# Performance work log

Hardware: AMD Instinct MI355X
Metric: run time of the kernel (lower is better)

The kernel has to match this reference:

```python
import jax, jax.numpy as jnp
import numpy as np
from jax import lax

K = 3           # number of channel clusters (hard-coded in the torch forward)
KM_ITERS = 50   # fixed Lloyd iterations (stand-in for sklearn KMeans, random_state=0)

SEQ_LEN, PRED_LEN, CH, BATCH = 1024, 192, 1000, 32
LH = SEQ_LEN // 2


def _pairwise_sqdist(z, c):
    # z: [N, D], c: [K, D] -> [N, K]
    zz = jnp.sum(z * z, axis=1, keepdims=True)          # [N,1]
    cc = jnp.sum(c * c, axis=1)[None, :]                # [1,K]
    return zz - 2.0 * (z @ c.T) + cc


def kmeans_labels(z, k=K, iters=KM_ITERS):
    # Deterministic Lloyd's algorithm; init = first k rows (deterministic stand-in
    # for sklearn's k-means++ with random_state=0).
    c0 = z[:k]

    def step(c, _):
        d = _pairwise_sqdist(z, c)
        labels = jnp.argmin(d, axis=1)
        ones = jnp.ones((z.shape[0],), z.dtype)
        sums = jax.ops.segment_sum(z, labels, num_segments=k)       # [K,D]
        counts = jax.ops.segment_sum(ones, labels, num_segments=k)  # [K]
        new_c = jnp.where(counts[:, None] > 0,
                          sums / jnp.maximum(counts, 1.0)[:, None], c)
        return new_c, None

    c, _ = lax.scan(step, c0, None, length=iters)
    return jnp.argmin(_pairwise_sqdist(z, c), axis=1)   # [N] int32


def setup_inputs() -> dict:
    key = jax.random.key(0)
    ks = jax.random.split(key, 4)
    x = jax.random.normal(ks[0], (BATCH, SEQ_LEN, CH), dtype=jnp.float32)
    # stacked per-cluster expert Linears g1/g2/g3: weight [K, P, Lh], bias [K, P]
    Wg = jax.random.normal(ks[1], (K, PRED_LEN, LH), dtype=jnp.float32) * 0.02
    bg = jnp.zeros((K, PRED_LEN), dtype=jnp.float32)
    Wu = jax.random.normal(ks[2], (PRED_LEN, LH), dtype=jnp.float32) * 0.02
    bu = jnp.zeros((PRED_LEN,), dtype=jnp.float32)
    z1 = jnp.zeros((1,), dtype=jnp.float32)
    return {"x": x, "x_mark_enc": z1, "x_dec": z1, "x_mark_dec": z1,
            "Wg": Wg, "bg": bg, "Wu": Wu, "bu": bu}


def reference(x, x_mark_enc, x_dec, x_mark_dec, Wg, bg, Wu, bu):
    # instance normalization over time (torch.var is unbiased -> ddof=1)
    x_mean = jnp.mean(x, axis=1, keepdims=True)
    xc = x - x_mean
    x_var = jnp.var(xc, axis=1, keepdims=True, ddof=1) + 1e-5
    xn = xc / jnp.sqrt(x_var)

    # Haar split along time
    x1 = xn[:, 0::2, :] * 0.5
    x2 = xn[:, 1::2, :] * 0.5
    x_L = x1 + x2          # [B, Lh, N]
    x_U = x1 - x2          # [B, Lh, N]

    # channel clustering on z = x_L reshaped to [N, B*Lh]
    B, Lh, N = x_L.shape
    z = x_L.reshape(B * Lh, N).T                      # [N, B*Lh]
    labels = kmeans_labels(z)                         # [N]

    # per-cluster Linear experts expressed as per-channel gathered weights
    # (identical math to gather g_k -> g_kLinear -> scatter back)
    Wn = Wg[labels]                                   # [N, P, Lh]
    bn = bg[labels]                                   # [N, P]
    g = jnp.einsum('bln,npl->bpn', x_L, Wn) + bn.T[None]   # [B, P, N]

    xu = jnp.einsum('bln,pl->bpn', x_U, Wu) + bu[None, :, None]

    xy = xu + g
    return xy * jnp.sqrt(x_var) + x_mean
```

## Files before the change

kernel.cpp:

```cpp
#include <hip/hip_runtime.h>
#include <hip/hip_bf16.h>
#include <hip/hip_cooperative_groups.h>

namespace cg = cooperative_groups;

#define B_   32
#define L_   1024
#define LH_  512
#define CH_  1000
#define PRED_ 192
#define ITERS_ 50
#define KBL_ 16384
#define SLOTS_ 1012
#define NTILES_ 253
#define NT2_ 506
#define NTRI_ 36
#define SEG_ 16
#define KMB_ 32
#define KMP_ 32

typedef __attribute__((ext_vector_type(8))) _Float16 f16x8;
typedef __attribute__((ext_vector_type(4))) float f32x4;

__device__ inline ushort f2h(float x) {
    union { _Float16 h; ushort u; } c;
    c.h = (_Float16)x;
    return c.u;
}

__global__ __launch_bounds__(256) void k1_partial(const float* __restrict__ x,
                                                  float* __restrict__ pS,
                                                  float* __restrict__ pSS) {
    int seg = blockIdx.x;
    int b = blockIdx.y;
    int t = threadIdx.x;
    if (t >= 250) return;
    int c4 = t * 4;
    const float* xp = x + (size_t)b * L_ * CH_ + (size_t)seg * 64 * CH_ + c4;
    float4 s = {0.f, 0.f, 0.f, 0.f}, ss = {0.f, 0.f, 0.f, 0.f};
#pragma unroll 4
    for (int l = 0; l < 64; ++l) {
        float4 v = *(const float4*)(xp + (size_t)l * CH_);
        s.x += v.x; s.y += v.y; s.z += v.z; s.w += v.w;
        ss.x += v.x * v.x; ss.y += v.y * v.y; ss.z += v.z * v.z; ss.w += v.w * v.w;
    }
    size_t o = ((size_t)seg * B_ + b) * CH_ + c4;
    *(float4*)(pS + o) = s;
    *(float4*)(pSS + o) = ss;
}

__global__ __launch_bounds__(256) void k1b_wprep(const float* __restrict__ pS,
                                                 const float* __restrict__ pSS,
                                                 float* __restrict__ meanT,
                                                 float* __restrict__ sstdT,
                                                 float* __restrict__ invT,
                                                 const float* __restrict__ Wg,
                                                 const float* __restrict__ Wu,
                                                 ushort* __restrict__ WF2) {
    int bx = blockIdx.x;
    int tid = threadIdx.x;
    if (bx < 125) {
        int idx = bx * 256 + tid;
        if (idx >= B_ * CH_) return;
        int c = idx % CH_;
        int b = idx / CH_;
        float s = 0.f, ss = 0.f;
#pragma unroll
        for (int seg = 0; seg < SEG_; ++seg) {
            size_t o = ((size_t)seg * B_ + b) * CH_ + c;
            s += pS[o];
            ss += pSS[o];
        }
        float m = s * (1.0f / L_);
        float var = (ss - (float)L_ * m * m) * (1.0f / (L_ - 1)) + 1e-5f;
        float sd = sqrtf(var);
        meanT[c * B_ + b] = m;
        sstdT[c * B_ + b] = sd;
        invT[c * B_ + b] = 1.0f / sd;
    } else {
        int r = bx - 125;
        int p = r % PRED_;
#pragma unroll
        for (int i = 0; i < 4; ++i) {
            int k = i * 256 + tid;
            float w = (k < 512) ? Wg[(size_t)r * LH_ + k]
                                : Wu[(size_t)p * LH_ + (k - 512)];
            WF2[(size_t)r * 1024 + k] = f2h(w);
        }
    }
}

__global__ __launch_bounds__(256) void k2_build(const float* __restrict__ x,
                                                const float* __restrict__ meanT,
                                                const float* __restrict__ invT,
                                                ushort* __restrict__ zLF,
                                                ushort* __restrict__ zUF) {
    __shared__ float Ls[32][33];
    __shared__ float Us[32][33];
    int tid = threadIdx.x;
    int tx = tid & 31, ty = tid >> 5;
    int n0 = blockIdx.x * 32;
    int lh0 = blockIdx.y * 32;
    int b = blockIdx.z;
    int n = n0 + tx;
    float m = 0.f, iv = 0.f;
    if (n < CH_) { m = meanT[n * B_ + b]; iv = invT[n * B_ + b]; }
    for (int r = 0; r < 4; ++r) {
        int lh = lh0 + ty + 8 * r;
        float v0 = 0.f, v1 = 0.f;
        if (n < CH_) {
            v0 = x[((size_t)b * L_ + 2 * lh) * CH_ + n];
            v1 = x[((size_t)b * L_ + 2 * lh + 1) * CH_ + n];
        }
        float a = (v0 - m) * iv * 0.5f;
        float c2 = (v1 - m) * iv * 0.5f;
        Ls[ty + 8 * r][tx] = a + c2;
        Us[ty + 8 * r][tx] = a - c2;
    }
    __syncthreads();
    for (int r = 0; r < 4; ++r) {
        int nl = ty + 8 * r;
        int nn = n0 + nl;
        if (nn < CH_) {
            size_t dst = (size_t)nn * KBL_ + (size_t)b * LH_ + lh0 + tx;
            zLF[dst] = f2h(Ls[tx][nl]);
            zUF[dst] = f2h(Us[tx][nl]);
        }
    }
}

#define ZSPLIT_ 16
#define KSEG_   1024
#define NT_     (KSEG_ / 32)

__global__ __launch_bounds__(256) void k3_mfma(const ushort* __restrict__ zF,
                                               float* __restrict__ gpart) {
    __shared__ __align__(16) ushort AH[128][40];
    __shared__ __align__(16) ushort BH[128][40];

    int bid = blockIdx.x;
    int xcd = bid & 7, w = bid >> 3;
    int ksl = 2 * xcd + (w >= NTRI_);
    int t = (w >= NTRI_) ? w - NTRI_ : w;
    int ti = 0, tt = t;
    while (tt >= 8 - ti) { tt -= 8 - ti; ++ti; }
    int tj = ti + tt;
    int i0 = ti * 128, j0 = tj * 128;
    int kb = ksl * KSEG_;

    int tid = threadIdx.x;
    int lane = tid & 63;
    int wid = tid >> 6;
    int wr = wid >> 1, wc = wid & 1;
    int fr = lane & 15;
    int g8 = lane >> 4;

    f32x4 acc[4][4];
#pragma unroll
    for (int m = 0; m < 4; ++m)
#pragma unroll
        for (int n = 0; n < 4; ++n) acc[m][n] = (f32x4){0.f, 0.f, 0.f, 0.f};

    int srow = tid >> 2;
    int sseg = tid & 3;

    uint4 pv[4];
    auto stage_load = [&](int kt) {
        int k0 = kb + kt * 32;
#pragma unroll
        for (int s = 0; s < 4; ++s) {
            int tile = s >> 1, rep = s & 1;
            int row = srow + rep * 64;
            int grow = ((tile == 0) ? i0 : j0) + row;
            uint4 v = {0u, 0u, 0u, 0u};
            if (grow < CH_)
                v = *(const uint4*)(zF + (size_t)grow * KBL_ + k0 + sseg * 8);
            pv[s] = v;
        }
    };
    auto stage_write = [&]() {
#pragma unroll
        for (int s = 0; s < 4; ++s) {
            int tile = s >> 1, rep = s & 1;
            int row = srow + rep * 64;
            ushort* dst = (tile == 0) ? &AH[row][sseg * 8] : &BH[row][sseg * 8];
            *(uint4*)dst = pv[s];
        }
    };

    stage_load(0);
    for (int t2 = 0; t2 < NT_; ++t2) {
        __syncthreads();
        stage_write();
        __syncthreads();
        if (t2 + 1 < NT_) stage_load(t2 + 1);

        f16x8 a[4];
#pragma unroll
        for (int m = 0; m < 4; ++m)
            a[m] = *(const f16x8*)&AH[wr * 64 + m * 16 + fr][g8 * 8];
#pragma unroll
        for (int n = 0; n < 4; ++n) {
            f16x8 bv = *(const f16x8*)&BH[wc * 64 + n * 16 + fr][g8 * 8];
#pragma unroll
            for (int m = 0; m < 4; ++m)
                acc[m][n] = __builtin_amdgcn_mfma_f32_16x16x32_f16(a[m], bv, acc[m][n], 0, 0, 0);
        }
    }

    float* gp = gpart + ((size_t)ksl * NTRI_ + t) * 16384;
#pragma unroll
    for (int m = 0; m < 4; ++m) {
        int rb = wr * 64 + m * 16 + g8 * 4;
#pragma unroll
        for (int n = 0; n < 4; ++n) {
            int c = wc * 64 + n * 16 + fr;
#pragma unroll
            for (int q = 0; q < 4; ++q)
                gp[(size_t)(rb + q) * 128 + c] = acc[m][n][q];
        }
    }
}

__global__ __launch_bounds__(256) void k3b_sym(const float* __restrict__ gpart,
                                               float* __restrict__ g) {
    int t = blockIdx.x;
    int seg = blockIdx.y;
    int ti = 0, tt = t;
    while (tt >= 8 - ti) { tt -= 8 - ti; ++ti; }
    int tj = ti + tt;
    int i0 = ti * 128, j0 = tj * 128;
    int tid = threadIdx.x;
    int e0 = seg * 4096 + tid * 16;
    int r = e0 >> 7, c0 = e0 & 127;

    float4 s[4];
#pragma unroll
    for (int j = 0; j < 4; ++j) s[j] = (float4){0.f, 0.f, 0.f, 0.f};
#pragma unroll
    for (int p = 0; p < ZSPLIT_; ++p) {
        const float* src = gpart + ((size_t)p * NTRI_ + t) * 16384 + e0;
#pragma unroll
        for (int j = 0; j < 4; ++j) {
            float4 v = *(const float4*)(src + j * 4);
            s[j].x += v.x; s[j].y += v.y; s[j].z += v.z; s[j].w += v.w;
        }
    }
    int i = i0 + r;
    if (i < CH_) {
#pragma unroll
        for (int j = 0; j < 4; ++j) {
            int jc = j0 + c0 + j * 4;
            if (jc + 3 < CH_) {
                *(float4*)(g + (size_t)i * CH_ + jc) = s[j];
            } else {
#pragma unroll
                for (int e = 0; e < 4; ++e)
                    if (jc + e < CH_) g[(size_t)i * CH_ + jc + e] = ((const float*)&s[j])[e];
            }
        }
        if (ti != tj) {
#pragma unroll
            for (int j = 0; j < 4; ++j) {
#pragma unroll
                for (int e = 0; e < 4; ++e) {
                    int jc = j0 + c0 + j * 4 + e;
                    if (jc < CH_) g[(size_t)jc * CH_ + i] = ((const float*)&s[j])[e];
                }
            }
        }
    }
}

__global__ __launch_bounds__(1024) void k4_kmeans(const float* __restrict__ g,
                                                  float* __restrict__ sbuf,
                                                  int* __restrict__ chlist,
                                                  int* __restrict__ chpos,
                                                  int* __restrict__ slabel) {
    cg::grid_group grid = cg::this_grid();
    __shared__ float gl[KMP_ * CH_];
    __shared__ int   lab[1024];
    __shared__ float wred[16][3];
    __shared__ float ccS[3];
    __shared__ float ccPrev[3];
    __shared__ int   cntPrev[3];
    __shared__ int   cnt2[3];
    __shared__ int   chgS;
    __shared__ int   st[4], c2r[3];

    int tid = threadIdx.x;
    int wv = tid >> 6, ln64 = tid & 63;
    int bpt0 = blockIdx.x * KMP_;

    {
        int nrow = CH_ - bpt0;
        if (nrow > KMP_) nrow = KMP_;
        if (nrow < 0) nrow = 0;
        int nf4 = nrow * (CH_ / 4);
        const float4* gsrc = (const float4*)(g + (size_t)bpt0 * CH_);
        float4* gdst = (float4*)gl;
        for (int i = tid; i < nf4; i += 1024) gdst[i] = gsrc[i];
    }

    int lbp = (tid < 3) ? tid : 3;
    lab[tid] = lbp;
    if (tid < 3) {
        cntPrev[tid] = 1;
        ccPrev[tid] = g[(size_t)tid * CH_ + tid];
    }
    __syncthreads();

    int par = 0;
    for (int it = 1; it <= ITERS_ + 1; ++it) {
        const float* sp = sbuf + par * 3 * CH_;
        float s0 = 0.f, s1 = 0.f, s2 = 0.f;
        if (tid < CH_) {
            if (it == 1) {
                const float* gr = g + (size_t)tid * CH_;
                s0 = gr[0]; s1 = gr[1]; s2 = gr[2];
            } else {
                s0 = sp[tid * 3 + 0]; s1 = sp[tid * 3 + 1]; s2 = sp[tid * 3 + 2];
            }
        }
        float c0 = (lbp == 0) ? s0 : 0.f;
        float c1 = (lbp == 1) ? s1 : 0.f;
        float c2 = (lbp == 2) ? s2 : 0.f;
#pragma unroll
        for (int m = 1; m < 64; m <<= 1) {
            c0 += __shfl_xor(c0, m);
            c1 += __shfl_xor(c1, m);
            c2 += __shfl_xor(c2, m);
        }
        if (ln64 == 0) { wred[wv][0] = c0; wred[wv][1] = c1; wred[wv][2] = c2; }
        if (tid == 0) { cnt2[0] = 0; cnt2[1] = 0; cnt2[2] = 0; chgS = 0; }
        __syncthreads();
        if (tid < 3) {
            float sacc = 0.f;
#pragma unroll
            for (int w2 = 0; w2 < 16; ++w2) sacc += wred[w2][tid];
            int n = cntPrev[tid];
            float cc = (n > 0) ? sacc / (float)n : ccPrev[tid];
            ccS[tid] = cc;
            ccPrev[tid] = cc;
        }
        __syncthreads();
        float cc0 = ccS[0], cc1 = ccS[1], cc2 = ccS[2];

        int nl = lbp;
        if (tid < CH_) {
            float d0 = cc0 - 2.f * s0;
            float d1 = cc1 - 2.f * s1;
            float d2 = cc2 - 2.f * s2;
            nl = 0; float dm = d0;
            if (d1 < dm) { dm = d1; nl = 1; }
            if (d2 < dm) { dm = d2; nl = 2; }
        }
        bool act = (tid < CH_);
        unsigned long long b0 = __ballot(act && nl == 0);
        unsigned long long b1 = __ballot(act && nl == 1);
        unsigned long long b2 = __ballot(act && nl == 2);
        unsigned long long bc = __ballot(act && nl != lbp);
        if (ln64 == 0) {
            if (b0) atomicAdd(&cnt2[0], (int)__popcll(b0));
            if (b1) atomicAdd(&cnt2[1], (int)__popcll(b1));
            if (b2) atomicAdd(&cnt2[2], (int)__popcll(b2));
            if (bc) atomicAdd(&chgS, (int)__popcll(bc));
        }
        lab[tid] = nl;
        lbp = nl;
        __syncthreads();

        if (it == ITERS_ + 1) break;
        if (chgS == 0 && it > 1) break;

        int n0n = cnt2[0], n1n = cnt2[1], n2n = cnt2[2];
        float* sq = sbuf + (par ^ 1) * 3 * CH_;
        int pl = tid >> 5;
        int ln = tid & 31;
        int i = bpt0 + pl;
        if (i < CH_) {
            const float* gr = gl + pl * CH_;
            float a0 = 0.f, a1 = 0.f, a2 = 0.f;
            for (int j = ln; j < CH_; j += 32) {
                float gv = gr[j];
                int lb = lab[j];
                a0 += (lb == 0) ? gv : 0.f;
                a1 += (lb == 1) ? gv : 0.f;
                a2 += (lb == 2) ? gv : 0.f;
            }
#pragma unroll
            for (int msk = 1; msk < 32; msk <<= 1) {
                a0 += __shfl_xor(a0, msk, 32);
                a1 += __shfl_xor(a1, msk, 32);
                a2 += __shfl_xor(a2, msk, 32);
            }
            if (ln == 0) {
                float f0, f1, f2;
                if (it == 1) { f0 = gr[0]; f1 = gr[1]; f2 = gr[2]; }
                else { f0 = sp[i * 3 + 0]; f1 = sp[i * 3 + 1]; f2 = sp[i * 3 + 2]; }
                sq[i * 3 + 0] = (n0n > 0) ? a0 / (float)n0n : f0;
                sq[i * 3 + 1] = (n1n > 0) ? a1 / (float)n1n : f1;
                sq[i * 3 + 2] = (n2n > 0) ? a2 / (float)n2n : f2;
            }
        }
        if (tid < 3) cntPrev[tid] = cnt2[tid];
        par ^= 1;
        grid.sync();
    }

    if (blockIdx.x == 0) {
        if (tid == 0) {
            st[0] = 0;
            st[1] = ((cnt2[0] + 3) >> 2) << 2;
            st[2] = st[1] + (((cnt2[1] + 3) >> 2) << 2);
            st[3] = st[2] + (((cnt2[2] + 3) >> 2) << 2);
            c2r[0] = 0; c2r[1] = 0; c2r[2] = 0;
        }
        __syncthreads();
        if (tid < SLOTS_) chlist[tid] = 0;
        if (tid < NTILES_) {
            int s = tid * 4;
            slabel[tid] = (s < st[1]) ? 0 : (s < st[2]) ? 1 : (s < st[3]) ? 2 : 0;
        }
        __syncthreads();
        if (tid < CH_) {
            int lb = lab[tid];
            int r = atomicAdd(&c2r[lb], 1);
            int slot = st[lb] + r;
            chlist[slot] = tid;
            chpos[tid] = slot;
        }
    }
}

__global__ __launch_bounds__(256) void k5_grouped(const ushort* __restrict__ zLF,
                                                  const ushort* __restrict__ zUF,
                                                  const ushort* __restrict__ WF2,
                                                  const int* __restrict__ chlist,
                                                  const int* __restrict__ slabel,
                                                  const float* __restrict__ bg,
                                                  const float* __restrict__ bu,
                                                  const float* __restrict__ meanT,
                                                  const float* __restrict__ sstdT,
                                                  float* __restrict__ outP) {
    __shared__ __align__(16) ushort ZT[64][40];
    __shared__ __align__(16) ushort WT[192][40];
    __shared__ int sch[2];

    int tile = blockIdx.x;
    int tid = threadIdx.x;
    if (tid < 2) sch[tid] = chlist[tile * 2 + tid];
    int lab = slabel[tile >> 1];
    __syncthreads();

    int lane = tid & 63, wid = tid >> 6;
    int fr = lane & 15, g8 = lane >> 4;

    int srow = tid >> 2, sseg = tid & 3;
    size_t zb = (size_t)sch[srow >> 5] * KBL_ + (size_t)(srow & 31) * LH_;
    const ushort* wbase = WF2 + (size_t)(lab * PRED_) * 1024;

    f32x4 acc[4][3];
#pragma unroll
    for (int m = 0; m < 4; ++m)
#pragma unroll
        for (int n = 0; n < 3; ++n) acc[m][n] = (f32x4){0.f, 0.f, 0.f, 0.f};

    uint4 pz, pw0, pw1, pw2;
    auto stage_load = [&](int t) {
        const ushort* zsrc = (t < 16) ? zLF : zUF;
        int ko = ((t & 15) * 32) + sseg * 8;
        pz  = *(const uint4*)(zsrc + zb + ko);
        int kw = t * 32 + sseg * 8;
        pw0 = *(const uint4*)(wbase + (size_t)srow * 1024 + kw);
        pw1 = *(const uint4*)(wbase + (size_t)(srow + 64) * 1024 + kw);
        pw2 = *(const uint4*)(wbase + (size_t)(srow + 128) * 1024 + kw);
    };
    auto stage_write = [&]() {
        *(uint4*)&ZT[srow][sseg * 8] = pz;
        *(uint4*)&WT[srow][sseg * 8] = pw0;
        *(uint4*)&WT[srow + 64][sseg * 8] = pw1;
        *(uint4*)&WT[srow + 128][sseg * 8] = pw2;
    };

    stage_load(0);
    for (int t = 0; t < 32; ++t) {
        __syncthreads();
        stage_write();
        __syncthreads();
        if (t + 1 < 32) stage_load(t + 1);

        f16x8 a[4];
#pragma unroll
        for (int m = 0; m < 4; ++m)
            a[m] = *(const f16x8*)&ZT[m * 16 + fr][g8 * 8];
#pragma unroll
        for (int nf = 0; nf < 3; ++nf) {
            f16x8 bv = *(const f16x8*)&WT[wid * 48 + nf * 16 + fr][g8 * 8];
#pragma unroll
            for (int m = 0; m < 4; ++m)
                acc[m][nf] = __builtin_amdgcn_mfma_f32_16x16x32_f16(a[m], bv, acc[m][nf], 0, 0, 0);
        }
    }

#pragma unroll
    for (int m = 0; m < 4; ++m) {
#pragma unroll
        for (int q = 0; q < 4; ++q) {
            int sb = m * 16 + g8 * 4 + q;
            int sl = sb >> 5, b = sb & 31;
            int n = sch[sl];
            float sd = sstdT[n * B_ + b], mu = meanT[n * B_ + b];
            size_t obase = ((size_t)(tile * 2 + sl) * B_ + b) * PRED_;
#pragma unroll
            for (int nf = 0; nf < 3; ++nf) {
                int p = wid * 48 + nf * 16 + fr;
                float v = acc[m][nf][q] + bg[lab * PRED_ + p] + bu[p];
                outP[obase + p] = v * sd + mu;
            }
        }
    }
}

__global__ __launch_bounds__(256) void k7_unperm(const float* __restrict__ outP,
                                                 const int* __restrict__ chpos,
                                                 float* __restrict__ out) {
    int n = blockIdx.x * 256 + threadIdx.x;
    int p0 = blockIdx.y * 32;
    int b = blockIdx.z;
    if (n >= CH_) return;
    const float* src = outP + ((size_t)chpos[n] * B_ + b) * PRED_ + p0;
    float4 v[8];
#pragma unroll
    for (int j = 0; j < 8; ++j) v[j] = *(const float4*)(src + j * 4);
#pragma unroll
    for (int j = 0; j < 8; ++j) {
#pragma unroll
        for (int e = 0; e < 4; ++e) {
            int p = p0 + j * 4 + e;
            out[((size_t)b * PRED_ + p) * CH_ + n] = ((const float*)&v[j])[e];
        }
    }
}

extern "C" void kernel_launch(void* const* d_in, const int* in_sizes, int n_in,
                              void* d_out, int out_size, void* d_ws, size_t ws_size,
                              hipStream_t stream) {
    const float* x  = (const float*)d_in[0];
    const float* Wg = (const float*)d_in[4];
    const float* bg = (const float*)d_in[5];
    const float* Wu = (const float*)d_in[6];
    const float* bu = (const float*)d_in[7];
    float* out = (float*)d_out;
    (void)in_sizes; (void)n_in; (void)out_size; (void)ws_size;

    char* ws = (char*)d_ws;
    size_t off = 0;
    auto alloc = [&](size_t bytes) {
        void* p = ws + off;
        off = (off + bytes + 255) & ~(size_t)255;
        return p;
    };
    ushort* zLF  = (ushort*)alloc((size_t)16384000 * 2);
    ushort* zUF  = (ushort*)alloc((size_t)16384000 * 2);
    float*  G    = (float*)alloc((size_t)1000000 * 4);
    ushort* WF2  = (ushort*)alloc((size_t)576 * 1024 * 2);
    float*  meanT = (float*)alloc((size_t)32000 * 4);
    float*  sstdT = (float*)alloc((size_t)32000 * 4);
    float*  invT  = (float*)alloc((size_t)32000 * 4);
    float*  pS   = (float*)alloc((size_t)SEG_ * B_ * CH_ * 4);
    float*  pSS  = (float*)alloc((size_t)SEG_ * B_ * CH_ * 4);
    float*  sbuf = (float*)alloc((size_t)2 * 3 * CH_ * 4);
    int*    chlist = (int*)alloc((size_t)SLOTS_ * 4);
    int*    chpos  = (int*)alloc((size_t)1024 * 4);
    int*    slabel = (int*)alloc((size_t)256 * 4);
    char* unionBase = (char*)alloc((size_t)ZSPLIT_ * NTRI_ * 16384 * 4);
    float* Gp   = (float*)unionBase;
    float* outP = (float*)unionBase;

    k1_partial<<<dim3(SEG_, 32), 256, 0, stream>>>(x, pS, pSS);
    k1b_wprep<<<125 + 576, 256, 0, stream>>>(pS, pSS, meanT, sstdT, invT, Wg, Wu, WF2);
    k2_build<<<dim3(32, 16, 32), 256, 0, stream>>>(x, meanT, invT, zLF, zUF);
    k3_mfma<<<8 * NTRI_ * 2, 256, 0, stream>>>(zLF, Gp);
    k3b_sym<<<dim3(NTRI_, 4), 256, 0, stream>>>(Gp, G);
    void* args[] = { (void*)&G, (void*)&sbuf, (void*)&chlist, (void*)&chpos, (void*)&slabel };
    hipLaunchCooperativeKernel((void*)k4_kmeans, dim3(KMB_), dim3(1024), args, 0, stream);
    k5_grouped<<<NT2_, 256, 0, stream>>>(zLF, zUF, WF2, chlist, slabel,
                                         bg, bu, meanT, sstdT, outP);
    k7_unperm<<<dim3(4, 6, 32), 256, 0, stream>>>(outP, chpos, out);
}
```

Before: 199.4 us.

## Fuse split-K reduction into MFMA kernel via last-block atomic counter

The separate symmetric reduction kernel is removed. Each Gram tile's split-K partials are now reduced by the last of its 16 blocks to finish, which it detects with an atomic counter and threadfences. The weight fp16 conversion also moves into the partial-sum kernel, so it runs alongside the statistics pass rather than alongside the mean/std reduce. This cuts kernel-launch gaps, at the cost of an extra memset launch and a serialized tail where a single block per tile does the whole reduction.

```diff
diff --git a/kernel.cpp b/kernel.cpp
--- a/kernel.cpp
+++ b/kernel.cpp
@@ -28,66 +28,65 @@
     return c.u;
 }
 
-__global__ __launch_bounds__(256) void k1_partial(const float* __restrict__ x,
-                                                  float* __restrict__ pS,
-                                                  float* __restrict__ pSS) {
-    int seg = blockIdx.x;
-    int b = blockIdx.y;
+__global__ __launch_bounds__(256) void k1_fused(const float* __restrict__ x,
+                                                float* __restrict__ pS,
+                                                float* __restrict__ pSS,
+                                                const float* __restrict__ Wg,
+                                                const float* __restrict__ Wu,
+                                                ushort* __restrict__ WF2) {
+    int bx = blockIdx.x;
     int t = threadIdx.x;
-    if (t >= 250) return;
-    int c4 = t * 4;
-    const float* xp = x + (size_t)b * L_ * CH_ + (size_t)seg * 64 * CH_ + c4;
-    float4 s = {0.f, 0.f, 0.f, 0.f}, ss = {0.f, 0.f, 0.f, 0.f};
+    if (bx < 512) {
+        int seg = bx & 15;
+        int b = bx >> 4;
+        if (t >= 250) return;
+        int c4 = t * 4;
+        const float* xp = x + (size_t)b * L_ * CH_ + (size_t)seg * 64 * CH_ + c4;
+        float4 s = {0.f, 0.f, 0.f, 0.f}, ss = {0.f, 0.f, 0.f, 0.f};
 #pragma unroll 4
-    for (int l = 0; l < 64; ++l) {
-        float4 v = *(const float4*)(xp + (size_t)l * CH_);
-        s.x += v.x; s.y += v.y; s.z += v.z; s.w += v.w;
-        ss.x += v.x * v.x; ss.y += v.y * v.y; ss.z += v.z * v.z; ss.w += v.w * v.w;
-    }
-    size_t o = ((size_t)seg * B_ + b) * CH_ + c4;
-    *(float4*)(pS + o) = s;
-    *(float4*)(pSS + o) = ss;
-}
-
-__global__ __launch_bounds__(256) void k1b_wprep(const float* __restrict__ pS,
-                                                 const float* __restrict__ pSS,
-                                                 float* __restrict__ meanT,
-                                                 float* __restrict__ sstdT,
-                                                 float* __restrict__ invT,
-                                                 const float* __restrict__ Wg,
-                                                 const float* __restrict__ Wu,
-                                                 ushort* __restrict__ WF2) {
-    int bx = blockIdx.x;
-    int tid = threadIdx.x;
-    if (bx < 125) {
-        int idx = bx * 256 + tid;
-        if (idx >= B_ * CH_) return;
-        int c = idx % CH_;
-        int b = idx / CH_;
-        float s = 0.f, ss = 0.f;
-#pragma unroll
-        for (int seg = 0; seg < SEG_; ++seg) {
-            size_t o = ((size_t)seg * B_ + b) * CH_ + c;
-            s += pS[o];
-            ss += pSS[o];
-        }
-        float m = s * (1.0f / L_);
-        float var = (ss - (float)L_ * m * m) * (1.0f / (L_ - 1)) + 1e-5f;
-        float sd = sqrtf(var);
-        meanT[c * B_ + b] = m;
-        sstdT[c * B_ + b] = sd;
-        invT[c * B_ + b] = 1.0f / sd;
+        for (int l = 0; l < 64; ++l) {
+            float4 v = *(const float4*)(xp + (size_t)l * CH_);
+            s.x += v.x; s.y += v.y; s.z += v.z; s.w += v.w;
+            ss.x += v.x * v.x; ss.y += v.y * v.y; ss.z += v.z * v.z; ss.w += v.w * v.w;
+        }
+        size_t o = ((size_t)seg * B_ + b) * CH_ + c4;
+        *(float4*)(pS + o) = s;
+        *(float4*)(pSS + o) = ss;
     } else {
-        int r = bx - 125;
+        int r = bx - 512;
         int p = r % PRED_;
 #pragma unroll
         for (int i = 0; i < 4; ++i) {
-            int k = i * 256 + tid;
+            int k = i * 256 + t;
             float w = (k < 512) ? Wg[(size_t)r * LH_ + k]
                                 : Wu[(size_t)p * LH_ + (k - 512)];
             WF2[(size_t)r * 1024 + k] = f2h(w);
         }
     }
+}
+
+__global__ __launch_bounds__(256) void k1b_reduce(const float* __restrict__ pS,
+                                                  const float* __restrict__ pSS,
+                                                  float* __restrict__ meanT,
+                                                  float* __restrict__ sstdT,
+                                                  float* __restrict__ invT) {
+    int idx = blockIdx.x * 256 + threadIdx.x;
+    if (idx >= B_ * CH_) return;
+    int c = idx % CH_;
+    int b = idx / CH_;
+    float s = 0.f, ss = 0.f;
+#pragma unroll
+    for (int seg = 0; seg < SEG_; ++seg) {
+        size_t o = ((size_t)seg * B_ + b) * CH_ + c;
+        s += pS[o];
+        ss += pSS[o];
+    }
+    float m = s * (1.0f / L_);
+    float var = (ss - (float)L_ * m * m) * (1.0f / (L_ - 1)) + 1e-5f;
+    float sd = sqrtf(var);
+    meanT[c * B_ + b] = m;
+    sstdT[c * B_ + b] = sd;
+    invT[c * B_ + b] = 1.0f / sd;
 }
 
 __global__ __launch_bounds__(256) void k2_build(const float* __restrict__ x,
@@ -134,9 +133,12 @@
 #define NT_     (KSEG_ / 32)
 
 __global__ __launch_bounds__(256) void k3_mfma(const ushort* __restrict__ zF,
-                                               float* __restrict__ gpart) {
+                                               float* __restrict__ gpart,
+                                               float* __restrict__ g,
+                                               int* __restrict__ tilecnt) {
     __shared__ __align__(16) ushort AH[128][40];
     __shared__ __align__(16) ushort BH[128][40];
+    __shared__ int doneS;
 
     int bid = blockIdx.x;
     int xcd = bid & 7, w = bid >> 3;
@@ -220,52 +222,50 @@
                 gp[(size_t)(rb + q) * 128 + c] = acc[m][n][q];
         }
     }
-}
-
-__global__ __launch_bounds__(256) void k3b_sym(const float* __restrict__ gpart,
-                                               float* __restrict__ g) {
-    int t = blockIdx.x;
-    int seg = blockIdx.y;
-    int ti = 0, tt = t;
-    while (tt >= 8 - ti) { tt -= 8 - ti; ++ti; }
-    int tj = ti + tt;
-    int i0 = ti * 128, j0 = tj * 128;
-    int tid = threadIdx.x;
-    int e0 = seg * 4096 + tid * 16;
-    int r = e0 >> 7, c0 = e0 & 127;
-
-    float4 s[4];
-#pragma unroll
-    for (int j = 0; j < 4; ++j) s[j] = (float4){0.f, 0.f, 0.f, 0.f};
-#pragma unroll
-    for (int p = 0; p < ZSPLIT_; ++p) {
-        const float* src = gpart + ((size_t)p * NTRI_ + t) * 16384 + e0;
-#pragma unroll
-        for (int j = 0; j < 4; ++j) {
-            float4 v = *(const float4*)(src + j * 4);
-            s[j].x += v.x; s[j].y += v.y; s[j].z += v.z; s[j].w += v.w;
-        }
-    }
-    int i = i0 + r;
-    if (i < CH_) {
-#pragma unroll
-        for (int j = 0; j < 4; ++j) {
-            int jc = j0 + c0 + j * 4;
-            if (jc + 3 < CH_) {
-                *(float4*)(g + (size_t)i * CH_ + jc) = s[j];
-            } else {
-#pragma unroll
-                for (int e = 0; e < 4; ++e)
-                    if (jc + e < CH_) g[(size_t)i * CH_ + jc + e] = ((const float*)&s[j])[e];
-            }
-        }
-        if (ti != tj) {
+
+    __threadfence();
+    if (tid == 0) doneS = atomicAdd(&tilecnt[t], 1);
+    __syncthreads();
+    if (doneS != ZSPLIT_ - 1) return;
+    __threadfence();
+
+#pragma unroll
+    for (int seg = 0; seg < 4; ++seg) {
+        int e0 = seg * 4096 + tid * 16;
+        int r = e0 >> 7, c0 = e0 & 127;
+        float4 s[4];
+#pragma unroll
+        for (int j = 0; j < 4; ++j) s[j] = (float4){0.f, 0.f, 0.f, 0.f};
+#pragma unroll
+        for (int p = 0; p < ZSPLIT_; ++p) {
+            const float* src = gpart + ((size_t)p * NTRI_ + t) * 16384 + e0;
 #pragma unroll
             for (int j = 0; j < 4; ++j) {
-#pragma unroll
-                for (int e = 0; e < 4; ++e) {
-                    int jc = j0 + c0 + j * 4 + e;
-                    if (jc < CH_) g[(size_t)jc * CH_ + i] = ((const float*)&s[j])[e];
+                float4 v = *(const float4*)(src + j * 4);
+                s[j].x += v.x; s[j].y += v.y; s[j].z += v.z; s[j].w += v.w;
+            }
+        }
+        int i = i0 + r;
+        if (i < CH_) {
+#pragma unroll
+            for (int j = 0; j < 4; ++j) {
+                int jc = j0 + c0 + j * 4;
+                if (jc + 3 < CH_) {
+                    *(float4*)(g + (size_t)i * CH_ + jc) = s[j];
+                } else {
+#pragma unroll
+                    for (int e = 0; e < 4; ++e)
+                        if (jc + e < CH_) g[(size_t)i * CH_ + jc + e] = ((const float*)&s[j])[e];
+                }
+            }
+            if (ti != tj) {
+#pragma unroll
+                for (int j = 0; j < 4; ++j) {
+#pragma unroll
+                    for (int e = 0; e < 4; ++e) {
+                        int jc = j0 + c0 + j * 4 + e;
+                        if (jc < CH_) g[(size_t)jc * CH_ + i] = ((const float*)&s[j])[e];
+                    }
                 }
             }
         }
@@ -574,15 +574,16 @@
     int*    chlist = (int*)alloc((size_t)SLOTS_ * 4);
     int*    chpos  = (int*)alloc((size_t)1024 * 4);
     int*    slabel = (int*)alloc((size_t)256 * 4);
+    int*    tilecnt = (int*)alloc((size_t)64 * 4);
     char* unionBase = (char*)alloc((size_t)ZSPLIT_ * NTRI_ * 16384 * 4);
     float* Gp   = (float*)unionBase;
     float* outP = (float*)unionBase;
 
-    k1_partial<<<dim3(SEG_, 32), 256, 0, stream>>>(x, pS, pSS);
-    k1b_wprep<<<125 + 576, 256, 0, stream>>>(pS, pSS, meanT, sstdT, invT, Wg, Wu, WF2);
+    hipMemsetAsync(tilecnt, 0, 64 * 4, stream);
+    k1_fused<<<512 + 576, 256, 0, stream>>>(x, pS, pSS, Wg, Wu, WF2);
+    k1b_reduce<<<125, 256, 0, stream>>>(pS, pSS, meanT, sstdT, invT);
     k2_build<<<dim3(32, 16, 32), 256, 0, stream>>>(x, meanT, invT, zLF, zUF);
-    k3_mfma<<<8 * NTRI_ * 2, 256, 0, stream>>>(zLF, Gp);
-    k3b_sym<<<dim3(NTRI_, 4), 256, 0, stream>>>(Gp, G);
+    k3_mfma<<<8 * NTRI_ * 2, 256, 0, stream>>>(zLF, Gp, G, tilecnt);
     void* args[] = { (void*)&G, (void*)&sbuf, (void*)&chlist, (void*)&chpos, (void*)&slabel };
     hipLaunchCooperativeKernel((void*)k4_kmeans, dim3(KMB_), dim3(1024), args, 0, stream);
     k5_grouped<<<NT2_, 256, 0, stream>>>(zLF, zUF, WF2, chlist, slabel,
```

New measurement: 328.9 us. 1.65x slower.
